# Optimization experiments

Hardware: AMD Instinct MI355X
Metric: run time of the kernel (lower is better)

Reference implementation:

```python
import jax, jax.numpy as jnp
import numpy as np


def _graph_conv_mean(x, src, dst, edge_weight, W_rel, W_root, b, num_nodes):
    # messages: gather source features, optionally scale by edge weight
    msg = x[src]  # [E, D]
    if edge_weight is not None:
        msg = msg * edge_weight[:, None]
    # mean aggregation over incoming edges per destination node
    summed = jax.ops.segment_sum(msg, dst, num_segments=num_nodes)  # [N, D]
    count = jax.ops.segment_sum(jnp.ones((src.shape[0],), x.dtype), dst, num_segments=num_nodes)
    mean = summed / jnp.maximum(count, 1.0)[:, None]
    # out = lin_rel(mean) + lin_root(x) + bias
    return mean @ W_rel + x @ W_root + b


def setup_inputs() -> dict:
    key = jax.random.key(0)
    ks = jax.random.split(key, 8)
    N, E, D, H, C = 100000, 1600000, 128, 32, 5
    x = jax.random.normal(ks[0], (N, D), dtype=jnp.float32)
    edge_index = jax.random.randint(ks[1], (2, E), 0, N, dtype=jnp.int64)
    edge_weight = jax.random.uniform(ks[2], (E,), dtype=jnp.float32)
    W_rel1 = jax.random.normal(ks[3], (D, H), dtype=jnp.float32) / np.sqrt(D)
    W_root1 = jax.random.normal(ks[4], (D, H), dtype=jnp.float32) / np.sqrt(D)
    b1 = jnp.zeros((H,), jnp.float32)
    W_rel2 = jax.random.normal(ks[5], (H, C), dtype=jnp.float32) / np.sqrt(H)
    W_root2 = jax.random.normal(ks[6], (H, C), dtype=jnp.float32) / np.sqrt(H)
    b2 = jnp.zeros((C,), jnp.float32)
    return {"x": x, "edge_index": edge_index, "edge_weight": edge_weight,
            "W_rel1": W_rel1, "W_root1": W_root1, "b1": b1,
            "W_rel2": W_rel2, "W_root2": W_root2, "b2": b2}


def reference(x, edge_index, edge_weight, W_rel1, W_root1, b1, W_rel2, W_root2, b2):
    N = x.shape[0]
    src, dst = edge_index[0], edge_index[1]
    # conv1 with edge_weight
    h = _graph_conv_mean(x, src, dst, edge_weight, W_rel1, W_root1, b1, N)
    h = jax.nn.relu(h)
    # dropout is identity at inference (training=False)
    # conv2 without edge_weight
    out = _graph_conv_mean(h, src, dst, None, W_rel2, W_root2, b2, N)
    return jax.nn.log_softmax(out, axis=1)
```

## Files before the change

kernel.cpp:

```cpp
#include <hip/hip_runtime.h>
#include <math.h>

#define N_NODES 100000
#define E_EDGES 1600000
#define D_IN    128
#define H_MID   32
#define C_OUT   5

#define NBKT   98
#define BSHIFT 10
#define BNODES 1024
#define BCAP   17500
#define SRC_BITS 17
#define SRC_MASK 0x1FFFF

#define KP 136

typedef __attribute__((ext_vector_type(8))) short bf16x8;
typedef __attribute__((ext_vector_type(4))) float f32x4;

__device__ inline unsigned f2bf(float f) {
    unsigned u = __float_as_uint(f);
    return (u + 0x7FFFu + ((u >> 16) & 1u)) >> 16;
}

__global__ __launch_bounds__(256) void k1_mfma(
    const float* __restrict__ x,
    const float* __restrict__ Wrel,
    const float* __restrict__ Wroot,
    const float* __restrict__ b1,
    unsigned short* __restrict__ xrelh,
    float* __restrict__ xroot) {
    __shared__ unsigned short xs[64 * KP];
    __shared__ unsigned short wt[64 * KP];
    int tid = threadIdx.x;
    int nodeBase = blockIdx.x * 64;

    #pragma unroll
    for (int it = 0; it < 32; ++it) {
        int idx = it * 256 + tid;
        int k = idx >> 6, n = idx & 63;
        float wvv = (n < 32) ? Wrel[k * H_MID + n] : Wroot[k * H_MID + (n - 32)];
        wt[n * KP + k] = (unsigned short)f2bf(wvv);
    }
    #pragma unroll
    for (int it = 0; it < 16; ++it) {
        int idx = it * 256 + tid;
        int row = idx >> 6, kp = idx & 63;
        int node = nodeBase + row;
        float2 v = make_float2(0.f, 0.f);
        if (node < N_NODES)
            v = *(const float2*)(x + (size_t)node * D_IN + kp * 2);
        unsigned pk = f2bf(v.x) | (f2bf(v.y) << 16);
        *(unsigned*)(xs + row * KP + kp * 2) = pk;
    }
    __syncthreads();

    int lane = tid & 63;
    int wv = tid >> 6;
    int m = lane & 15;
    int quad = lane >> 4;

    f32x4 acc[4];
    #pragma unroll
    for (int nt = 0; nt < 4; ++nt) acc[nt] = (f32x4){0.f, 0.f, 0.f, 0.f};

    #pragma unroll
    for (int kk = 0; kk < 4; ++kk) {
        int k0 = kk * 32 + quad * 8;
        bf16x8 a = *(const bf16x8*)(xs + (wv * 16 + m) * KP + k0);
        #pragma unroll
        for (int nt = 0; nt < 4; ++nt) {
            bf16x8 b = *(const bf16x8*)(wt + (nt * 16 + m) * KP + k0);
            acc[nt] = __builtin_amdgcn_mfma_f32_16x16x32_bf16(a, b, acc[nt], 0, 0, 0);
        }
    }

    #pragma unroll
    for (int nt = 0; nt < 4; ++nt) {
        #pragma unroll
        for (int r = 0; r < 4; ++r) {
            int node = nodeBase + wv * 16 + quad * 4 + r;
            int colg = nt * 16 + m;
            if (node < N_NODES) {
                if (colg < H_MID) {
                    xrelh[(size_t)node * H_MID + colg] =
                        (unsigned short)f2bf(acc[nt][r]);
                } else {
                    int c = colg - H_MID;
                    xroot[(size_t)node * H_MID + c] = acc[nt][r] + b1[c];
                }
            }
        }
    }
}

__global__ void k_zero_small(int* __restrict__ p, int n) {
    int i = threadIdx.x;
    if (i < n) p[i] = 0;
}

__global__ __launch_bounds__(1024) void k_binA(
    const int* __restrict__ src,
    const int* __restrict__ dst,
    const float* __restrict__ ew,
    int* __restrict__ bucket_cursor,
    int2* __restrict__ staged) {
    __shared__ int cnt[NBKT];
    __shared__ int lstart[NBKT];
    __shared__ int gbase[NBKT];
    __shared__ int scanbuf[128];
    __shared__ int2 ebuf[1024];
    __shared__ short bbuf[1024];
    int tid = threadIdx.x;
    int e = blockIdx.x * 1024 + tid;

    if (tid < NBKT) cnt[tid] = 0;
    __syncthreads();

    int b = 0, rank = 0, packed = 0, wbits = 0;
    bool valid = (e < E_EDGES);
    if (valid) {
        int d = dst[e];
        int s = src[e];
        wbits = __float_as_int(ew[e]);
        b = d >> BSHIFT;
        packed = ((d & (BNODES - 1)) << SRC_BITS) | s;
        rank = atomicAdd(&cnt[b], 1);
    }
    __syncthreads();

    if (tid < 128) scanbuf[tid] = (tid < NBKT) ? cnt[tid] : 0;
    __syncthreads();
    for (int off = 1; off < 128; off <<= 1) {
        int t = 0;
        if (tid < 128 && tid >= off) t = scanbuf[tid - off];
        __syncthreads();
        if (tid < 128) scanbuf[tid] += t;
        __syncthreads();
    }
    if (tid < NBKT) {
        lstart[tid] = scanbuf[tid] - cnt[tid];
        gbase[tid]  = atomicAdd(&bucket_cursor[tid], cnt[tid]);
    }
    __syncthreads();
    int total = scanbuf[NBKT - 1];

    if (valid) {
        int slot = lstart[b] + rank;
        ebuf[slot] = make_int2(packed, wbits);
        bbuf[slot] = (short)b;
    }
    __syncthreads();

    if (tid < total) {
        int2 ev = ebuf[tid];
        int bb = bbuf[tid];
        int gpos = gbase[bb] + (tid - lstart[bb]);
        if (gpos < BCAP)
            staged[(size_t)bb * BCAP + gpos] = ev;
    }
}

__global__ void k_bktscan(const int* __restrict__ bucket_cursor,
                          int* __restrict__ bucket_base) {
    __shared__ int s[128];
    int i = threadIdx.x;
    int c = (i < NBKT) ? bucket_cursor[i] : 0;
    int v = (c > BCAP) ? BCAP : c;
    s[i] = v;
    __syncthreads();
    for (int off = 1; off < 128; off <<= 1) {
        int t = (i >= off) ? s[i - off] : 0;
        __syncthreads();
        s[i] += t;
        __syncthreads();
    }
    if (i < NBKT) bucket_base[i] = s[i] - v;
}

__global__ __launch_bounds__(1024) void k_binB2(
    const int* __restrict__ bucket_cursor,
    const int* __restrict__ bucket_base,
    const int2* __restrict__ staged,
    int* __restrict__ deg,
    int* __restrict__ offsets,
    int2* __restrict__ csr8) {
    __shared__ int hist[BNODES];
    __shared__ int scanb[BNODES];
    __shared__ int cur[BNODES];
    int tid = threadIdx.x;
    int b = blockIdx.x;
    int count = bucket_cursor[b];
    if (count > BCAP) count = BCAP;
    int base = bucket_base[b];
    int nodeBase = b << BSHIFT;
    const int2* sp = staged + (size_t)b * BCAP;

    hist[tid] = 0;
    __syncthreads();

    for (int i = tid; i < count; i += 1024)
        atomicAdd(&hist[((unsigned)sp[i].x) >> SRC_BITS], 1);
    __syncthreads();

    int v = hist[tid];
    scanb[tid] = v;
    __syncthreads();
    for (int off = 1; off < BNODES; off <<= 1) {
        int t = (tid >= off) ? scanb[tid - off] : 0;
        __syncthreads();
        scanb[tid] += t;
        __syncthreads();
    }
    int excl = scanb[tid] - v;
    int node = nodeBase + tid;
    if (node < N_NODES) {
        deg[node]     = v;
        offsets[node] = base + excl;
    }
    cur[tid] = excl;
    __syncthreads();

    for (int i = tid; i < count; i += 1024) {
        int2 ev = sp[i];
        int local = ((unsigned)ev.x) >> SRC_BITS;
        int pos = atomicAdd(&cur[local], 1);
        csr8[base + pos] = make_int2(ev.x & SRC_MASK, ev.y);
    }
}

__global__ __launch_bounds__(256) void k_layer1(
    const int* __restrict__ offsets,
    const int* __restrict__ deg,
    const int2* __restrict__ csr8,
    const unsigned short* __restrict__ xrelh,
    const float* __restrict__ xroot,
    const float* __restrict__ Wrel2,
    const float* __restrict__ Wroot2,
    const float* __restrict__ b2,
    float* __restrict__ h2rel,
    float* __restrict__ h2root) {
    int node = blockIdx.x * 16 + (threadIdx.x >> 4);
    int lane = threadIdx.x & 15;
    int beg = offsets[node];
    int dg  = deg[node];
    int end = beg + dg;

    float acc0 = 0.f, acc1 = 0.f;
    int i = beg;
    for (; i + 8 <= end; i += 8) {
        int2 e[8];
        unsigned v[8];
        #pragma unroll
        for (int u = 0; u < 8; ++u) e[u] = csr8[i + u];
        #pragma unroll
        for (int u = 0; u < 8; ++u)
            v[u] = *(const unsigned*)(xrelh + (size_t)e[u].x * H_MID + lane * 2);
        #pragma unroll
        for (int u = 0; u < 8; ++u) {
            float w = __int_as_float(e[u].y);
            acc0 += __uint_as_float((v[u] & 0xFFFFu) << 16) * w;
            acc1 += __uint_as_float(v[u] & 0xFFFF0000u) * w;
        }
    }
    for (; i < end; ++i) {
        int2 e0 = csr8[i];
        unsigned v0 = *(const unsigned*)(xrelh + (size_t)e0.x * H_MID + lane * 2);
        float w0 = __int_as_float(e0.y);
        acc0 += __uint_as_float((v0 & 0xFFFFu) << 16) * w0;
        acc1 += __uint_as_float(v0 & 0xFFFF0000u) * w0;
    }

    float inv = 1.0f / fmaxf((float)dg, 1.0f);
    float2 rt = *(const float2*)(xroot + (size_t)node * H_MID + lane * 2);
    float h0 = fmaxf(acc0 * inv + rt.x, 0.f);
    float h1 = fmaxf(acc1 * inv + rt.y, 0.f);

    float p[2 * C_OUT];
    #pragma unroll
    for (int j = 0; j < C_OUT; ++j) {
        p[j]         = h0 * Wrel2[(2 * lane) * C_OUT + j]
                     + h1 * Wrel2[(2 * lane + 1) * C_OUT + j];
        p[C_OUT + j] = h0 * Wroot2[(2 * lane) * C_OUT + j]
                     + h1 * Wroot2[(2 * lane + 1) * C_OUT + j];
    }
    #pragma unroll
    for (int mm = 8; mm > 0; mm >>= 1) {
        #pragma unroll
        for (int j = 0; j < 2 * C_OUT; ++j)
            p[j] += __shfl_xor(p[j], mm, 16);
    }
    if (lane == 0) {
        #pragma unroll
        for (int j = 0; j < C_OUT; ++j) {
            h2rel[(size_t)node * C_OUT + j]  = p[j];
            h2root[(size_t)node * C_OUT + j] = p[C_OUT + j] + b2[j];
        }
    }
}

__global__ __launch_bounds__(256) void k_layer2(
    const int* __restrict__ offsets,
    const int* __restrict__ deg,
    const int2* __restrict__ csr8,
    const float* __restrict__ h2rel,
    const float* __restrict__ h2root,
    float* __restrict__ out) {
    int node = blockIdx.x * 32 + (threadIdx.x >> 3);
    int lane = threadIdx.x & 7;
    int beg = offsets[node];
    int dg  = deg[node];
    int end = beg + dg;

    float acc = 0.f;
    if (lane < C_OUT) {
        int i = beg;
        for (; i + 8 <= end; i += 8) {
            int s[8];
            float v[8];
            #pragma unroll
            for (int u = 0; u < 8; ++u) s[u] = csr8[i + u].x;
            #pragma unroll
            for (int u = 0; u < 8; ++u)
                v[u] = h2rel[(size_t)s[u] * C_OUT + lane];
            #pragma unroll
            for (int u = 0; u < 8; ++u) acc += v[u];
        }
        for (; i < end; ++i)
            acc += h2rel[(size_t)csr8[i].x * C_OUT + lane];
    }
    float inv = 1.0f / fmaxf((float)dg, 1.0f);
    float o = (lane < C_OUT)
                  ? acc * inv + h2root[(size_t)node * C_OUT + lane]
                  : -INFINITY;
    float m = o;
    #pragma unroll
    for (int dd = 4; dd > 0; dd >>= 1) m = fmaxf(m, __shfl_xor(m, dd, 8));
    float e = (lane < C_OUT) ? expf(o - m) : 0.f;
    float ssum = e;
    #pragma unroll
    for (int dd = 4; dd > 0; dd >>= 1) ssum += __shfl_xor(ssum, dd, 8);
    float lse = m + logf(ssum);
    if (lane < C_OUT)
        out[(size_t)node * C_OUT + lane] = o - lse;
}

extern "C" void kernel_launch(void* const* d_in, const int* in_sizes, int n_in,
                              void* d_out, int out_size, void* d_ws, size_t ws_size,
                              hipStream_t stream) {
    const float* x      = (const float*)d_in[0];
    const int*   ei     = (const int*)d_in[1];
    const float* ew     = (const float*)d_in[2];
    const float* Wrel1  = (const float*)d_in[3];
    const float* Wroot1 = (const float*)d_in[4];
    const float* b1     = (const float*)d_in[5];
    const float* Wrel2  = (const float*)d_in[6];
    const float* Wroot2 = (const float*)d_in[7];
    const float* b2     = (const float*)d_in[8];
    float* out = (float*)d_out;

    const int* src = ei;
    const int* dst = ei + E_EDGES;

    char* ws = (char*)d_ws;
    int*   deg           = (int*)ws;
    int*   bucket_cursor = deg + N_NODES;
    int*   bucket_base   = bucket_cursor + 128;
    int*   offsets       = bucket_base + 128;
    int2*  csr8          = (int2*)(offsets + N_NODES);
    unsigned short* xrelh = (unsigned short*)(csr8 + E_EDGES);
    float* xroot         = (float*)(xrelh + (size_t)N_NODES * H_MID);
    float* h2rel         = xroot + (size_t)N_NODES * H_MID;
    float* h2root        = h2rel + (size_t)N_NODES * C_OUT;
    int2*  staged        = (int2*)xrelh;

    k_zero_small<<<1, 128, 0, stream>>>(bucket_cursor, 128);
    k_binA<<<(E_EDGES + 1023) / 1024, 1024, 0, stream>>>(src, dst, ew,
                                                         bucket_cursor, staged);
    k_bktscan<<<1, 128, 0, stream>>>(bucket_cursor, bucket_base);
    k_binB2<<<NBKT, 1024, 0, stream>>>(bucket_cursor, bucket_base, staged,
                                       deg, offsets, csr8);

    k1_mfma<<<(N_NODES + 63) / 64, 256, 0, stream>>>(x, Wrel1, Wroot1, b1,
                                                     xrelh, xroot);

    k_layer1<<<N_NODES / 16, 256, 0, stream>>>(offsets, deg, csr8,
                                               xrelh, xroot, Wrel2, Wroot2, b2,
                                               h2rel, h2root);

    k_layer2<<<N_NODES / 32, 256, 0, stream>>>(offsets, deg, csr8,
                                               h2rel, h2root, out);
}
```

Measured before the change: 244.8 us.

## Fuse small prep kernels, precompute bf16 weights, and double edges per binning block

```diff
diff --git a/kernel.cpp b/kernel.cpp
--- a/kernel.cpp
+++ b/kernel.cpp
@@ -24,25 +24,29 @@
     return (u + 0x7FFFu + ((u >> 16) & 1u)) >> 16;
 }
 
+__global__ void k_prep(const float* __restrict__ Wrel,
+                       const float* __restrict__ Wroot,
+                       int* __restrict__ bucket_cursor,
+                       unsigned short* __restrict__ wt_g) {
+    int tid = threadIdx.x;
+    if (tid < 128) bucket_cursor[tid] = 0;
+    for (int i = tid; i < 64 * 128; i += 256) {
+        int n = i >> 7, k = i & 127;
+        float v = (n < H_MID) ? Wrel[k * H_MID + n] : Wroot[k * H_MID + (n - H_MID)];
+        wt_g[i] = (unsigned short)f2bf(v);
+    }
+}
+
 __global__ __launch_bounds__(256) void k1_mfma(
     const float* __restrict__ x,
-    const float* __restrict__ Wrel,
-    const float* __restrict__ Wroot,
+    const unsigned short* __restrict__ wt_g,
     const float* __restrict__ b1,
     unsigned short* __restrict__ xrelh,
     float* __restrict__ xroot) {
     __shared__ unsigned short xs[64 * KP];
-    __shared__ unsigned short wt[64 * KP];
     int tid = threadIdx.x;
     int nodeBase = blockIdx.x * 64;
 
-    #pragma unroll
-    for (int it = 0; it < 32; ++it) {
-        int idx = it * 256 + tid;
-        int k = idx >> 6, n = idx & 63;
-        float wvv = (n < 32) ? Wrel[k * H_MID + n] : Wroot[k * H_MID + (n - 32)];
-        wt[n * KP + k] = (unsigned short)f2bf(wvv);
-    }
     #pragma unroll
     for (int it = 0; it < 16; ++it) {
         int idx = it * 256 + tid;
@@ -71,7 +75,7 @@
         bf16x8 a = *(const bf16x8*)(xs + (wv * 16 + m) * KP + k0);
         #pragma unroll
         for (int nt = 0; nt < 4; ++nt) {
-            bf16x8 b = *(const bf16x8*)(wt + (nt * 16 + m) * KP + k0);
+            bf16x8 b = *(const bf16x8*)(wt_g + (nt * 16 + m) * 128 + k0);
             acc[nt] = __builtin_amdgcn_mfma_f32_16x16x32_bf16(a, b, acc[nt], 0, 0, 0);
         }
     }
@@ -95,11 +99,6 @@
     }
 }
 
-__global__ void k_zero_small(int* __restrict__ p, int n) {
-    int i = threadIdx.x;
-    if (i < n) p[i] = 0;
-}
-
 __global__ __launch_bounds__(1024) void k_binA(
     const int* __restrict__ src,
     const int* __restrict__ dst,
@@ -110,23 +109,29 @@
     __shared__ int lstart[NBKT];
     __shared__ int gbase[NBKT];
     __shared__ int scanbuf[128];
-    __shared__ int2 ebuf[1024];
-    __shared__ short bbuf[1024];
+    __shared__ int2 ebuf[2048];
+    __shared__ short bbuf[2048];
     int tid = threadIdx.x;
-    int e = blockIdx.x * 1024 + tid;
+    int eBase = blockIdx.x * 2048;
 
     if (tid < NBKT) cnt[tid] = 0;
     __syncthreads();
 
-    int b = 0, rank = 0, packed = 0, wbits = 0;
-    bool valid = (e < E_EDGES);
-    if (valid) {
-        int d = dst[e];
-        int s = src[e];
-        wbits = __float_as_int(ew[e]);
-        b = d >> BSHIFT;
-        packed = ((d & (BNODES - 1)) << SRC_BITS) | s;
-        rank = atomicAdd(&cnt[b], 1);
+    int b[2], rank[2], packed[2], wbits[2];
+    bool valid[2];
+    #pragma unroll
+    for (int u = 0; u < 2; ++u) {
+        int e = eBase + u * 1024 + tid;
+        valid[u] = (e < E_EDGES);
+        b[u] = 0; rank[u] = 0; packed[u] = 0; wbits[u] = 0;
+        if (valid[u]) {
+            int d = dst[e];
+            int s = src[e];
+            wbits[u] = __float_as_int(ew[e]);
+            b[u] = d >> BSHIFT;
+            packed[u] = ((d & (BNODES - 1)) << SRC_BITS) | s;
+            rank[u] = atomicAdd(&cnt[b[u]], 1);
+        }
     }
     __syncthreads();
 
@@ -146,42 +151,27 @@
     __syncthreads();
     int total = scanbuf[NBKT - 1];
 
-    if (valid) {
-        int slot = lstart[b] + rank;
-        ebuf[slot] = make_int2(packed, wbits);
-        bbuf[slot] = (short)b;
-    }
-    __syncthreads();
-
-    if (tid < total) {
-        int2 ev = ebuf[tid];
-        int bb = bbuf[tid];
-        int gpos = gbase[bb] + (tid - lstart[bb]);
+    #pragma unroll
+    for (int u = 0; u < 2; ++u) {
+        if (valid[u]) {
+            int slot = lstart[b[u]] + rank[u];
+            ebuf[slot] = make_int2(packed[u], wbits[u]);
+            bbuf[slot] = (short)b[u];
+        }
+    }
+    __syncthreads();
+
+    for (int t = tid; t < total; t += 1024) {
+        int2 ev = ebuf[t];
+        int bb = bbuf[t];
+        int gpos = gbase[bb] + (t - lstart[bb]);
         if (gpos < BCAP)
             staged[(size_t)bb * BCAP + gpos] = ev;
     }
 }
 
-__global__ void k_bktscan(const int* __restrict__ bucket_cursor,
-                          int* __restrict__ bucket_base) {
-    __shared__ int s[128];
-    int i = threadIdx.x;
-    int c = (i < NBKT) ? bucket_cursor[i] : 0;
-    int v = (c > BCAP) ? BCAP : c;
-    s[i] = v;
-    __syncthreads();
-    for (int off = 1; off < 128; off <<= 1) {
-        int t = (i >= off) ? s[i - off] : 0;
-        __syncthreads();
-        s[i] += t;
-        __syncthreads();
-    }
-    if (i < NBKT) bucket_base[i] = s[i] - v;
-}
-
 __global__ __launch_bounds__(1024) void k_binB2(
     const int* __restrict__ bucket_cursor,
-    const int* __restrict__ bucket_base,
     const int2* __restrict__ staged,
     int* __restrict__ deg,
     int* __restrict__ offsets,
@@ -189,16 +179,28 @@
     __shared__ int hist[BNODES];
     __shared__ int scanb[BNODES];
     __shared__ int cur[BNODES];
+    __shared__ int sbase[128];
     int tid = threadIdx.x;
     int b = blockIdx.x;
+
+    if (tid < 128) {
+        int c = (tid < NBKT) ? bucket_cursor[tid] : 0;
+        sbase[tid] = (c > BCAP) ? BCAP : c;
+    }
+    hist[tid] = 0;
+    __syncthreads();
+    for (int off = 1; off < 128; off <<= 1) {
+        int t = 0;
+        if (tid < 128 && tid >= off) t = sbase[tid - off];
+        __syncthreads();
+        if (tid < 128) sbase[tid] += t;
+        __syncthreads();
+    }
     int count = bucket_cursor[b];
     if (count > BCAP) count = BCAP;
-    int base = bucket_base[b];
+    int base = sbase[b] - count;
     int nodeBase = b << BSHIFT;
     const int2* sp = staged + (size_t)b * BCAP;
-
-    hist[tid] = 0;
-    __syncthreads();
 
     for (int i = tid; i < count; i += 1024)
         atomicAdd(&hist[((unsigned)sp[i].x) >> SRC_BITS], 1);
@@ -366,8 +368,8 @@
     char* ws = (char*)d_ws;
     int*   deg           = (int*)ws;
     int*   bucket_cursor = deg + N_NODES;
-    int*   bucket_base   = bucket_cursor + 128;
-    int*   offsets       = bucket_base + 128;
+    unsigned short* wt_g = (unsigned short*)(bucket_cursor + 128);
+    int*   offsets       = (int*)(wt_g + 64 * 128);
     int2*  csr8          = (int2*)(offsets + N_NODES);
     unsigned short* xrelh = (unsigned short*)(csr8 + E_EDGES);
     float* xroot         = (float*)(xrelh + (size_t)N_NODES * H_MID);
@@ -375,14 +377,14 @@
     float* h2root        = h2rel + (size_t)N_NODES * C_OUT;
     int2*  staged        = (int2*)xrelh;
 
-    k_zero_small<<<1, 128, 0, stream>>>(bucket_cursor, 128);
-    k_binA<<<(E_EDGES + 1023) / 1024, 1024, 0, stream>>>(src, dst, ew,
+    k_prep<<<1, 256, 0, stream>>>(Wrel1, Wroot1, bucket_cursor, wt_g);
+
+    k_binA<<<(E_EDGES + 2047) / 2048, 1024, 0, stream>>>(src, dst, ew,
                                                          bucket_cursor, staged);
-    k_bktscan<<<1, 128, 0, stream>>>(bucket_cursor, bucket_base);
-    k_binB2<<<NBKT, 1024, 0, stream>>>(bucket_cursor, bucket_base, staged,
+    k_binB2<<<NBKT, 1024, 0, stream>>>(bucket_cursor, staged,
                                        deg, offsets, csr8);
 
-    k1_mfma<<<(N_NODES + 63) / 64, 256, 0, stream>>>(x, Wrel1, Wroot1, b1,
+    k1_mfma<<<(N_NODES + 63) / 64, 256, 0, stream>>>(x, wt_g, b1,
                                                      xrelh, xroot);
 
     k_layer1<<<N_NODES / 16, 256, 0, stream>>>(offsets, deg, csr8,
```

New measurement: 231.2 us. 5.6% less time.
